# Kernel tuning notes

Measured on AMD Instinct MI355X. Metric: run time of the kernel, lower is better.

Reference implementation:

```python
import jax, jax.numpy as jnp
import numpy as np

B, S, D, M = 8, 32, 256, 2048
TOPK = 8

def setup_inputs() -> dict:
    key = jax.random.key(0)
    ks = jax.random.split(key, 10)
    def lin(kw, fan_in, fan_out):
        # kaiming normal (linear): std = 1/sqrt(fan_in); stored as [in, out]
        return jax.random.normal(kw, (fan_in, fan_out), jnp.float32) / jnp.sqrt(fan_in)
    return {
        "x": jax.random.normal(ks[0], (B, S, D), jnp.float32),
        "memory": jax.random.normal(ks[1], (M, D), jnp.float32) * 0.02,
        "Wq": lin(ks[2], D, D), "bq": jnp.zeros((D,), jnp.float32),
        "Wk": lin(ks[3], D, D), "bk": jnp.zeros((D,), jnp.float32),
        "Wv": lin(ks[4], D, D), "bv": jnp.zeros((D,), jnp.float32),
        "Wg": lin(ks[5], 2 * D, D), "bg": jnp.zeros((D,), jnp.float32),
    }

def reference(x, memory, Wq, bq, Wk, bk, Wv, bv, Wg, bg):
    batch, seq_len, d = x.shape
    scale = jnp.sqrt(jnp.float32(d))
    mem0 = jnp.broadcast_to(memory[None], (batch,) + memory.shape)  # [B,M,D]
    b_idx = jnp.arange(batch)[:, None]

    def step(mem, xt):  # mem [B,M,D], xt [B,D]
        q = xt @ Wq + bq                      # [B,D]
        k = mem @ Wk + bk                     # [B,M,D]
        v = mem @ Wv + bv                     # [B,M,D]
        logits = jnp.einsum('bd,bmd->bm', q, k) / scale
        attn = jax.nn.softmax(logits, axis=-1)            # [B,M]
        out = jnp.einsum('bm,bmd->bd', attn, v)           # [B,D]
        g = jax.nn.sigmoid(jnp.concatenate([xt, out], axis=-1) @ Wg + bg)  # [B,D]
        _, top_idx = jax.lax.top_k(attn, TOPK)            # [B,TOPK]
        old = jnp.take_along_axis(mem, top_idx[:, :, None], axis=1)        # [B,TOPK,D]
        new = (1.0 - g)[:, None, :] * old + g[:, None, :] * xt[:, None, :]
        mem = mem.at[b_idx, top_idx].set(new)
        return mem, out

    _, outs = jax.lax.scan(step, mem0, jnp.swapaxes(x, 0, 1))  # outs [S,B,D]
    return jnp.swapaxes(outs, 0, 1)  # [B,S,D]
```

## Files before the change

### kernel.cpp

```cpp
#include <hip/hip_runtime.h>
#include <math.h>

constexpr int B_ = 8, S_ = 32, D_ = 256, M_ = 2048;
constexpr int N_ = S_ * B_;
constexpr int TK = 8;
constexpr int NSLOT = 256;
constexpr int TOPC = 256;
constexpr int NCAND = NSLOT + TOPC;
constexpr int KSPLIT = 4;
constexpr int CACHE0 = 192;

__global__ __launch_bounds__(256) void k_wvwgT(const float* __restrict__ Wv,
                                               const float* __restrict__ Wg,
                                               const float* __restrict__ bv,
                                               const float* __restrict__ bg,
                                               const float* __restrict__ Wk,
                                               float* __restrict__ WvWgB,
                                               float* __restrict__ bvg,
                                               float* __restrict__ WkT) {
  int blk = blockIdx.x;
  int tid = threadIdx.x;
  if (blk >= 17) {
    __shared__ float tile[32][33];
    int bb = blk - 17;
    int bx = bb & 7, by = bb >> 3;
    int x0 = bx * 32, y0 = by * 32;
    int tx = tid & 31, ty = tid >> 5;
    for (int j = ty; j < 32; j += 8) tile[j][tx] = Wk[(y0 + j) * D_ + x0 + tx];
    __syncthreads();
    for (int j = ty; j < 32; j += 8) WkT[(x0 + j) * D_ + y0 + tx] = tile[tx][j];
    return;
  }
  if (blk == 16) {
    float a = bg[tid];
#pragma unroll 8
    for (int j = 0; j < D_; ++j) a = fmaf(bv[j], Wg[(size_t)(D_ + j) * D_ + tid], a);
    bvg[tid] = a;
    return;
  }
  int i0 = (blk & 3) * 64, d0 = (blk >> 2) * 64;
  __shared__ float At[64 * 64];
  __shared__ float Bt[64 * 64];
  const int r = tid & 63, c = tid >> 6;
  const int lane = tid & 63, wvv = tid >> 6;
  const int tx = lane & 15, ty = lane >> 4;
  const int dg = tx * 4, ig = (wvv * 4 + ty) * 4;
  float acc[4][4];
#pragma unroll
  for (int i = 0; i < 4; ++i)
#pragma unroll
    for (int j = 0; j < 4; ++j) acc[i][j] = 0.f;
  for (int kc = 0; kc < 4; ++kc) {
    __syncthreads();
#pragma unroll
    for (int it = 0; it < 4; ++it) {
      int jq = (c * 4 + it) * 4;
      float4 a = *(const float4*)&Wv[(i0 + r) * D_ + kc * 64 + jq];
      At[(jq + 0) * 64 + r] = a.x; At[(jq + 1) * 64 + r] = a.y;
      At[(jq + 2) * 64 + r] = a.z; At[(jq + 3) * 64 + r] = a.w;
      *(float4*)&Bt[r * 64 + jq] =
          *(const float4*)&Wg[(size_t)(D_ + kc * 64 + r) * D_ + d0 + jq];
    }
    __syncthreads();
#pragma unroll 4
    for (int j = 0; j < 64; ++j) {
      float4 av = *(const float4*)&At[j * 64 + ig];
      float4 bv4 = *(const float4*)&Bt[j * 64 + dg];
      acc[0][0] = fmaf(av.x, bv4.x, acc[0][0]); acc[0][1] = fmaf(av.x, bv4.y, acc[0][1]);
      acc[0][2] = fmaf(av.x, bv4.z, acc[0][2]); acc[0][3] = fmaf(av.x, bv4.w, acc[0][3]);
      acc[1][0] = fmaf(av.y, bv4.x, acc[1][0]); acc[1][1] = fmaf(av.y, bv4.y, acc[1][1]);
      acc[1][2] = fmaf(av.y, bv4.z, acc[1][2]); acc[1][3] = fmaf(av.y, bv4.w, acc[1][3]);
      acc[2][0] = fmaf(av.z, bv4.x, acc[2][0]); acc[2][1] = fmaf(av.z, bv4.y, acc[2][1]);
      acc[2][2] = fmaf(av.z, bv4.z, acc[2][2]); acc[2][3] = fmaf(av.z, bv4.w, acc[2][3]);
      acc[3][0] = fmaf(av.w, bv4.x, acc[3][0]); acc[3][1] = fmaf(av.w, bv4.y, acc[3][1]);
      acc[3][2] = fmaf(av.w, bv4.z, acc[3][2]); acc[3][3] = fmaf(av.w, bv4.w, acc[3][3]);
    }
  }
#pragma unroll
  for (int i = 0; i < 4; ++i)
    *(float4*)&WvWgB[(size_t)(i0 + ig + i) * D_ + d0 + dg] =
        make_float4(acc[i][0], acc[i][1], acc[i][2], acc[i][3]);
}

__global__ __launch_bounds__(256) void k_qproj(
    const float* __restrict__ x, const float* __restrict__ Wq,
    const float* __restrict__ bq, const float* __restrict__ bk,
    const float* __restrict__ WkT, const float* __restrict__ Wg,
    float* __restrict__ qt, float* __restrict__ qbk, float* __restrict__ xgp) {
  int n = blockIdx.x, tid = threadIdx.x;
  int t = n / B_, b = n % B_;
  __shared__ float xr[D_], qsh[D_];
  __shared__ float red[4];
  xr[tid] = x[(b * S_ + t) * D_ + tid];
  __syncthreads();
  float accq = bq[tid], accg = 0.f;
#pragma unroll 8
  for (int i = 0; i < D_; ++i) {
    float xv = xr[i];
    accq = fmaf(xv, Wq[i * D_ + tid], accq);
    accg = fmaf(xv, Wg[i * D_ + tid], accg);
  }
  qsh[tid] = accq;
  xgp[n * D_ + tid] = accg;
  float p = accq * bk[tid];
  for (int off = 32; off > 0; off >>= 1) p += __shfl_down(p, off, 64);
  if ((tid & 63) == 0) red[tid >> 6] = p;
  __syncthreads();
  float acct = 0.f;
#pragma unroll 8
  for (int i = 0; i < D_; ++i) acct = fmaf(qsh[i], WkT[i * D_ + tid], acct);
  qt[n * D_ + tid] = acct;
  if (tid == 0) qbk[n] = red[0] + red[1] + red[2] + red[3];
}

__global__ __launch_bounds__(256) void k_L0(
    const float* __restrict__ qt, const float* __restrict__ mem,
    const float* __restrict__ qbk, float* __restrict__ L0) {
  __shared__ float qtT[64 * 64];
  __shared__ float mT[64 * 64];
  const int tid = threadIdx.x;
  const int m0 = blockIdx.x * 64, n0 = blockIdx.y * 64;
  const int r = tid & 63, c = tid >> 6;
  const int lane = tid & 63, wv = tid >> 6;
  const int tx = lane & 15, ty = lane >> 4;
  const int mg = tx * 4, ng = (wv * 4 + ty) * 4;
  float acc[4][4];
#pragma unroll
  for (int i = 0; i < 4; ++i)
#pragma unroll
    for (int j = 0; j < 4; ++j) acc[i][j] = 0.f;
  for (int kc = 0; kc < 4; ++kc) {
    __syncthreads();
#pragma unroll
    for (int it = 0; it < 4; ++it) {
      int kq = (c * 4 + it) * 4;
      float4 a = *(const float4*)&qt[(n0 + r) * D_ + kc * 64 + kq];
      qtT[(kq + 0) * 64 + r] = a.x; qtT[(kq + 1) * 64 + r] = a.y;
      qtT[(kq + 2) * 64 + r] = a.z; qtT[(kq + 3) * 64 + r] = a.w;
      float4 bm = *(const float4*)&mem[(m0 + r) * D_ + kc * 64 + kq];
      mT[(kq + 0) * 64 + r] = bm.x; mT[(kq + 1) * 64 + r] = bm.y;
      mT[(kq + 2) * 64 + r] = bm.z; mT[(kq + 3) * 64 + r] = bm.w;
    }
    __syncthreads();
#pragma unroll 4
    for (int k = 0; k < 64; ++k) {
      float4 av = *(const float4*)&qtT[k * 64 + ng];
      float4 bv4 = *(const float4*)&mT[k * 64 + mg];
      acc[0][0] = fmaf(av.x, bv4.x, acc[0][0]); acc[0][1] = fmaf(av.x, bv4.y, acc[0][1]);
      acc[0][2] = fmaf(av.x, bv4.z, acc[0][2]); acc[0][3] = fmaf(av.x, bv4.w, acc[0][3]);
      acc[1][0] = fmaf(av.y, bv4.x, acc[1][0]); acc[1][1] = fmaf(av.y, bv4.y, acc[1][1]);
      acc[1][2] = fmaf(av.y, bv4.z, acc[1][2]); acc[1][3] = fmaf(av.y, bv4.w, acc[1][3]);
      acc[2][0] = fmaf(av.z, bv4.x, acc[2][0]); acc[2][1] = fmaf(av.z, bv4.y, acc[2][1]);
      acc[2][2] = fmaf(av.z, bv4.z, acc[2][2]); acc[2][3] = fmaf(av.z, bv4.w, acc[2][3]);
      acc[3][0] = fmaf(av.w, bv4.x, acc[3][0]); acc[3][1] = fmaf(av.w, bv4.y, acc[3][1]);
      acc[3][2] = fmaf(av.w, bv4.z, acc[3][2]); acc[3][3] = fmaf(av.w, bv4.w, acc[3][3]);
    }
  }
#pragma unroll
  for (int i = 0; i < 4; ++i) {
    int n = n0 + ng + i;
    float qbv = qbk[n];
    float4 o;
    o.x = (acc[i][0] + qbv) * 0.0625f; o.y = (acc[i][1] + qbv) * 0.0625f;
    o.z = (acc[i][2] + qbv) * 0.0625f; o.w = (acc[i][3] + qbv) * 0.0625f;
    *(float4*)&L0[n * M_ + m0 + mg] = o;
  }
}

__global__ __launch_bounds__(1024) void k_sortstats(const float* __restrict__ L0,
                                                    float* __restrict__ topv,
                                                    int* __restrict__ topi,
                                                    float* __restrict__ M0,
                                                    double* __restrict__ SumE0) {
  int n = blockIdx.x, tid = threadIdx.x;
  __shared__ float v[M_];
  __shared__ short ix[M_];
  __shared__ double redd[16];
  for (int m = tid; m < M_; m += 1024) {
    v[m] = L0[(size_t)n * M_ + m];
    ix[m] = (short)m;
  }
  __syncthreads();
  for (int size = 2; size <= M_; size <<= 1) {
    for (int stride = size >> 1; stride > 0; stride >>= 1) {
      const int i = tid;
      const int pos = 2 * i - (i & (stride - 1));
      const int j = pos + stride;
      const bool desc = ((pos & size) == 0);
      const float va = v[pos], vb2 = v[j];
      const short ia = ix[pos], ib = ix[j];
      const bool aG = (va > vb2) || (va == vb2 && ia < ib);
      if (desc ? !aG : aG) { v[pos] = vb2; v[j] = va; ix[pos] = ib; ix[j] = ia; }
      __syncthreads();
    }
  }
  if (tid < TOPC) {
    topv[n * TOPC + tid] = v[tid];
    topi[n * TOPC + tid] = (int)ix[tid];
  }
  float mx = v[0];
  if (tid == 0) M0[n] = mx;
  double s = 0.0;
  for (int m = tid; m < M_; m += 1024) s += (double)expf(v[m] - mx);
  for (int off = 32; off > 0; off >>= 1) s += __shfl_down(s, off, 64);
  if ((tid & 63) == 0) redd[tid >> 6] = s;
  __syncthreads();
  if (tid == 0) {
    double t = 0.0;
#pragma unroll
    for (int w = 0; w < 16; ++w) t += redd[w];
    SumE0[n] = t;
  }
}

__global__ __launch_bounds__(256) void k_ctxpart(
    const float* __restrict__ L0, const float* __restrict__ M0,
    const float* __restrict__ mem, float* __restrict__ ctxp) {
  int ks = blockIdx.x;
  int n0 = blockIdx.y * 32;
  int d0 = blockIdx.z * 64;
  int tid = threadIdx.x;
  __shared__ float Et[64 * 32];
  __shared__ float mTl[64 * 64];
  __shared__ float Msh[32];
  if (tid < 32) Msh[tid] = M0[n0 + tid];
  const int lane = tid & 63, wv = tid >> 6;
  const int tx = lane & 15, ty = lane >> 4;
  const int ng = (wv * 4 + ty) * 2;
  const int dg = tx * 4;
  float acc[2][4] = {{0, 0, 0, 0}, {0, 0, 0, 0}};
  for (int kc = 0; kc < 8; ++kc) {
    int kb = ks * 512 + kc * 64;
    __syncthreads();
#pragma unroll
    for (int j = 0; j < 8; ++j) {
      int ii = tid + 256 * j;
      int nr = ii & 31, kk = ii >> 5;
      Et[kk * 32 + nr] = expf(L0[(n0 + nr) * M_ + kb + kk] - Msh[nr]);
    }
    {
      int r = tid & 63, c = tid >> 6;
#pragma unroll
      for (int j = 0; j < 4; ++j) {
        int c4 = (c * 4 + j) * 4;
        *(float4*)&mTl[r * 64 + c4] = *(const float4*)&mem[(kb + r) * D_ + d0 + c4];
      }
    }
    __syncthreads();
#pragma unroll 4
    for (int kk = 0; kk < 64; ++kk) {
      float4 mv = *(const float4*)&mTl[kk * 64 + dg];
      float e0v = Et[kk * 32 + ng], e1v = Et[kk * 32 + ng + 1];
      acc[0][0] = fmaf(e0v, mv.x, acc[0][0]); acc[0][1] = fmaf(e0v, mv.y, acc[0][1]);
      acc[0][2] = fmaf(e0v, mv.z, acc[0][2]); acc[0][3] = fmaf(e0v, mv.w, acc[0][3]);
      acc[1][0] = fmaf(e1v, mv.x, acc[1][0]); acc[1][1] = fmaf(e1v, mv.y, acc[1][1]);
      acc[1][2] = fmaf(e1v, mv.z, acc[1][2]); acc[1][3] = fmaf(e1v, mv.w, acc[1][3]);
    }
  }
#pragma unroll
  for (int i = 0; i < 2; ++i) {
    int n = n0 + ng + i;
    *(float4*)&ctxp[((size_t)ks * N_ + n) * D_ + d0 + dg] =
        make_float4(acc[i][0], acc[i][1], acc[i][2], acc[i][3]);
  }
}

__device__ __forceinline__ unsigned long long shfl_xor_u64(unsigned long long v,
                                                           int off) {
  const int lo = __shfl_xor((int)(unsigned)(v & 0xFFFFFFFFull), off, 64);
  const int hi = __shfl_xor((int)(unsigned)(v >> 32), off, 64);
  return ((unsigned long long)(unsigned)hi << 32) | (unsigned)lo;
}

#define CE8(i, jj)                                                  \
  {                                                                 \
    const unsigned long long ka_ = key[i], kb_ = key[jj];           \
    const bool sw_ = kb_ > ka_;                                     \
    key[i] = sw_ ? kb_ : ka_;                                       \
    key[jj] = sw_ ? ka_ : kb_;                                      \
  }

__global__ __launch_bounds__(1024, 4) void k_scan(
    const float* __restrict__ x, const float* __restrict__ mem0,
    const float* __restrict__ Wv, const float* __restrict__ bv,
    const float* __restrict__ WvWgB, const float* __restrict__ bvg,
    const float* __restrict__ qt, const float* __restrict__ qbk,
    const float* __restrict__ xgp, const float* __restrict__ L0,
    const float* __restrict__ M0, const double* __restrict__ SumE0,
    const float* __restrict__ ctxp, const float* __restrict__ topv,
    const int* __restrict__ topi, float* __restrict__ memcur,
    float* __restrict__ out) {
  const int b = blockIdx.x;
  const int tid = threadIdx.x;
  const int lane = tid & 63;
  const int wvid = tid >> 6;

  __shared__ short tpos[M_];
  __shared__ unsigned int descL[NSLOT];
  __shared__ __align__(16) float candV[NCAND];
  __shared__ __align__(16) int candI[NCAND];
  __shared__ float diffA[NSLOT];
  __shared__ float dpart[15][D_];
  __shared__ float fpart[15][D_];
  __shared__ float fpart2[15][D_];
  __shared__ float qt_s[2][D_], xt_s[2][D_];
  __shared__ float CTX0_s[D_], xgp_s[D_], g_s[D_], bv_s[D_], bvg_s[D_];
  __shared__ float wvlds[(256 - CACHE0) * D_];
  __shared__ float Msc[S_], qbks[S_];
  __shared__ double sum0s[S_];
  __shared__ float inv_esum;
  __shared__ int Tcount;

  const float4* mem04 = (const float4*)mem0;
  const float4* mcur4c = (const float4*)memcur;
  float4* mcur4 = (float4*)memcur;
  const float4* Wv4 = (const float4*)Wv;
  const float4* Wg4 = (const float4*)WvWgB;
  const float4* qt4 = (const float4*)qt;
  const float4* x4 = (const float4*)x;
  const float4* ctxp4 = (const float4*)ctxp;
  const float4* xgp4 = (const float4*)xgp;
  const float4* wvlds4 = (const float4*)wvlds;

  float4 wreg[18];
  {
    const int kbase = 17 * wvid;
    if (wvid < 15) {
#pragma unroll
      for (int j = 0; j < 17; ++j) wreg[j] = Wv4[(size_t)(kbase + j) * 64 + lane];
      wreg[17] = (wvid == 14) ? Wv4[(size_t)255 * 64 + lane] : wreg[16];
    }
  }

  for (int m = tid; m < M_; m += 1024) tpos[m] = -1;
  for (int s = tid; s < NSLOT; s += 1024) descL[s] = 0;
  for (int i = tid; i < (256 - CACHE0) * 64; i += 1024)
    ((float4*)wvlds)[i] = Wg4[(size_t)CACHE0 * 64 + i];
  if (tid < NCAND) {
    candV[tid] = -INFINITY;
    candI[tid] = 0x7FFFFFFF;
  }
  if (tid < S_) {
    Msc[tid] = M0[tid * B_ + b];
    qbks[tid] = qbk[tid * B_ + b];
    sum0s[tid] = SumE0[tid * B_ + b];
  } else if (tid >= 64 && tid < 64 + D_) {
    int d = tid - 64;
    bv_s[d] = bv[d];
    bvg_s[d] = bvg[d];
  } else if (tid >= 512 && tid < 576) {
    int j = tid - 512;
    ((float4*)qt_s[0])[j] = qt4[(size_t)b * 64 + j];
  } else if (tid >= 576 && tid < 640) {
    int j = tid - 576;
    ((float4*)xt_s[0])[j] = x4[(size_t)(b * S_) * 64 + j];
  }
  if (tid == 0) Tcount = 0;
  __syncthreads();

  for (int t = 0; t < S_; ++t) {
    const int n = t * B_ + b;
    const int par = t & 1;
    const int Tc = Tcount;
    const float c0 = Msc[t];
    const float qb = qbks[t];

    if (wvid < 15) {
      const float4 qv = ((const float4*)qt_s[par])[lane];
      const float4 g4 = ((const float4*)g_s)[lane];
      const float4 xpv = ((const float4*)xt_s[par ^ 1])[lane];
      float4 acc = make_float4(0.f, 0.f, 0.f, 0.f);
      int s = wvid;
      unsigned int dsc_c = 0;
      float4 mc_c = make_float4(0.f, 0.f, 0.f, 0.f), mo_c = mc_c;
      float l0_c = 0.f;
      if (s < Tc) {
        dsc_c = descL[s];
        const int m = dsc_c & 2047;
        mo_c = mem04[(size_t)m * 64 + lane];
        const bool fromM0 = (dsc_c & (1u << 12)) && (dsc_c & (1u << 11));
        mc_c = fromM0 ? mo_c : mcur4c[(size_t)(b * NSLOT + s) * 64 + lane];
        l0_c = L0[(size_t)n * M_ + m];
      }
      while (s < Tc) {
        const int s2 = s + 15;
        unsigned int dsc_n = 0;
        float4 mc_n = make_float4(0.f, 0.f, 0.f, 0.f), mo_n = mc_n;
        float l0_n = 0.f;
        if (s2 < Tc) {
          dsc_n = descL[s2];
          const int mn = dsc_n & 2047;
          mo_n = mem04[(size_t)mn * 64 + lane];
          const bool fromM0n = (dsc_n & (1u << 12)) && (dsc_n & (1u << 11));
          mc_n = fromM0n ? mo_n : mcur4c[(size_t)(b * NSLOT + s2) * 64 + lane];
          l0_n = L0[(size_t)n * M_ + mn];
        }
        const int m = dsc_c & 2047;
        if (dsc_c & (1u << 12)) {
          mc_c.x = fmaf(g4.x, xpv.x - mc_c.x, mc_c.x);
          mc_c.y = fmaf(g4.y, xpv.y - mc_c.y, mc_c.y);
          mc_c.z = fmaf(g4.z, xpv.z - mc_c.z, mc_c.z);
          mc_c.w = fmaf(g4.w, xpv.w - mc_c.w, mc_c.w);
          mcur4[(size_t)(b * NSLOT + s) * 64 + lane] = mc_c;
          if (lane == 0) descL[s] = (unsigned int)m;
        }
        float p = mc_c.x * qv.x;
        p = fmaf(mc_c.y, qv.y, p);
        p = fmaf(mc_c.z, qv.z, p);
        p = fmaf(mc_c.w, qv.w, p);
#pragma unroll
        for (int off = 1; off < 64; off <<= 1) p += __shfl_xor(p, off, 64);
        const float cur = (p + qb) * 0.0625f;
        const float ce = expf(cur - c0);
        const float e0 = expf(l0_c - c0);
        acc.x = fmaf(ce, mc_c.x, fmaf(-e0, mo_c.x, acc.x));
        acc.y = fmaf(ce, mc_c.y, fmaf(-e0, mo_c.y, acc.y));
        acc.z = fmaf(ce, mc_c.z, fmaf(-e0, mo_c.z, acc.z));
        acc.w = fmaf(ce, mc_c.w, fmaf(-e0, mo_c.w, acc.w));
        if (lane == 0) {
          diffA[s] = ce - e0;
          candV[s] = cur;
          candI[s] = m;
        }
        dsc_c = dsc_n;
        mc_c = mc_n;
        mo_c = mo_n;
        l0_c = l0_n;
        s = s2;
      }
      ((float4*)dpart[wvid])[lane] = acc;
    } else {
#pragma unroll
      for (int jj = 0; jj < 4; ++jj) {
        const int j = lane + jj * 64;
        const int ii = topi[n * TOPC + j];
        const bool fresh = (tpos[ii] < 0);
        candV[NSLOT + j] = fresh ? topv[n * TOPC + j] : -INFINITY;
        candI[NSLOT + j] = fresh ? ii : 0x7FFFFFFF;
      }
      const float4 c0v = ctxp4[(size_t)(0 * N_ + n) * 64 + lane];
      const float4 c1v = ctxp4[(size_t)(1 * N_ + n) * 64 + lane];
      const float4 c2v = ctxp4[(size_t)(2 * N_ + n) * 64 + lane];
      const float4 c3v = ctxp4[(size_t)(3 * N_ + n) * 64 + lane];
      ((float4*)CTX0_s)[lane] = make_float4(c0v.x + c1v.x + c2v.x + c3v.x,
                                            c0v.y + c1v.y + c2v.y + c3v.y,
                                            c0v.z + c1v.z + c2v.z + c3v.z,
                                            c0v.w + c1v.w + c2v.w + c3v.w);
      ((float4*)xgp_s)[lane] = xgp4[(size_t)n * 64 + lane];
      if (t + 1 < S_) {
        ((float4*)qt_s[par ^ 1])[lane] = qt4[(size_t)(n + B_) * 64 + lane];
        ((float4*)xt_s[par ^ 1])[lane] = x4[(size_t)(b * S_ + t + 1) * 64 + lane];
      }
    }
    __syncthreads();

    if (wvid < 15) {
      const int kbase = 17 * wvid;
      const int nr = (wvid == 14) ? 18 : 17;
      float mynum = 0.f;
      if (lane < nr) {
        const int k = (lane == 17) ? 255 : (kbase + lane);
        float nv = CTX0_s[k];
#pragma unroll
        for (int p = 0; p < 15; ++p) nv += dpart[p][k];
        mynum = nv;
      }
      float4 a1 = make_float4(0.f, 0.f, 0.f, 0.f);
      float4 a2 = make_float4(0.f, 0.f, 0.f, 0.f);
#pragma unroll
      for (int j = 0; j < 17; ++j) {
        const float nv = __int_as_float(__builtin_amdgcn_readlane(__float_as_int(mynum), j));
        a1.x = fmaf(nv, wreg[j].x, a1.x); a1.y = fmaf(nv, wreg[j].y, a1.y);
        a1.z = fmaf(nv, wreg[j].z, a1.z); a1.w = fmaf(nv, wreg[j].w, a1.w);
        const int r = kbase + j;
        const float4 w4 = (r >= CACHE0) ? wvlds4[(size_t)(r - CACHE0) * 64 + lane]
                                        : Wg4[(size_t)r * 64 + lane];
        a2.x = fmaf(nv, w4.x, a2.x); a2.y = fmaf(nv, w4.y, a2.y);
        a2.z = fmaf(nv, w4.z, a2.z); a2.w = fmaf(nv, w4.w, a2.w);
      }
      if (wvid == 14) {
        const float nv = __int_as_float(__builtin_amdgcn_readlane(__float_as_int(mynum), 17));
        a1.x = fmaf(nv, wreg[17].x, a1.x); a1.y = fmaf(nv, wreg[17].y, a1.y);
        a1.z = fmaf(nv, wreg[17].z, a1.z); a1.w = fmaf(nv, wreg[17].w, a1.w);
        const float4 w4 = wvlds4[(size_t)(255 - CACHE0) * 64 + lane];
        a2.x = fmaf(nv, w4.x, a2.x); a2.y = fmaf(nv, w4.y, a2.y);
        a2.z = fmaf(nv, w4.z, a2.z); a2.w = fmaf(nv, w4.w, a2.w);
      }
      ((float4*)fpart[wvid])[lane] = a1;
      ((float4*)fpart2[wvid])[lane] = a2;
      if (wvid == 0) {
        double dsum = 0.0;
        for (int s2 = lane; s2 < Tc; s2 += 64) dsum += (double)diffA[s2];
#pragma unroll
        for (int off = 32; off > 0; off >>= 1) dsum += __shfl_down(dsum, off, 64);
        if (lane == 0) inv_esum = (float)(1.0 / (sum0s[t] + dsum));
      }
    } else if (t + 1 < S_) {
      const float4 cv0 = ((const float4*)candV)[lane * 2];
      const float4 cv1 = ((const float4*)candV)[lane * 2 + 1];
      const int4 ci0 = ((const int4*)candI)[lane * 2];
      const int4 ci1 = ((const int4*)candI)[lane * 2 + 1];
      unsigned long long key[8];
      {
        const float vs[8] = {cv0.x, cv0.y, cv0.z, cv0.w, cv1.x, cv1.y, cv1.z, cv1.w};
        const int is[8] = {ci0.x, ci0.y, ci0.z, ci0.w, ci1.x, ci1.y, ci1.z, ci1.w};
#pragma unroll
        for (int j = 0; j < 8; ++j) {
          unsigned int bits = __float_as_uint(vs[j]);
          bits = (bits & 0x80000000u) ? ~bits : (bits | 0x80000000u);
          key[j] = ((unsigned long long)bits << 11) |
                   (unsigned long long)(2047 - (is[j] & 2047));
        }
      }
      CE8(0, 1) CE8(2, 3) CE8(4, 5) CE8(6, 7)
      CE8(0, 2) CE8(1, 3) CE8(4, 6) CE8(5, 7)
      CE8(1, 2) CE8(5, 6)
      CE8(0, 4) CE8(1, 5) CE8(2, 6) CE8(3, 7)
      CE8(2, 4) CE8(3, 5)
      CE8(1, 2) CE8(3, 4) CE8(5, 6)
#pragma unroll
      for (int off = 1; off < 64; off <<= 1) {
        unsigned long long pk[8];
#pragma unroll
        for (int j = 0; j < 8; ++j) pk[j] = shfl_xor_u64(key[7 - j], off);
#pragma unroll
        for (int j = 0; j < 8; ++j) key[j] = (pk[j] > key[j]) ? pk[j] : key[j];
        CE8(0, 4) CE8(1, 5) CE8(2, 6) CE8(3, 7)
        CE8(0, 2) CE8(1, 3) CE8(4, 6) CE8(5, 7)
        CE8(0, 1) CE8(2, 3) CE8(4, 5) CE8(6, 7)
      }
      int myM = 2047 - (int)(key[0] & 2047);
#pragma unroll
      for (int r = 1; r < TK; ++r) {
        const int mr = 2047 - (int)(key[r] & 2047);
        if (lane == r) myM = mr;
      }
      int sOld = 0;
      bool fresh = false;
      if (lane < TK) {
        sOld = (int)tpos[myM];
        fresh = sOld < 0;
      }
      const unsigned long long fm = __ballot(fresh);
      if (lane < TK) {
        const int before = (int)__popcll(fm & ((1ull << lane) - 1ull));
        const int snew = fresh ? (Tc + before) : sOld;
        if (fresh) {
          tpos[myM] = (short)snew;
          candI[snew] = myM;
        }
        descL[snew] = (unsigned int)myM | ((fresh ? 1u : 0u) << 11) | (1u << 12);
      }
      if (lane == 0) Tcount = Tc + (int)__popcll(fm);
    }
    __syncthreads();

    if (tid < D_) {
      float o = 0.f;
#pragma unroll
      for (int p = 0; p < 15; ++p) o += fpart[p][tid];
      o = o * inv_esum + bv_s[tid];
      out[((size_t)b * S_ + t) * D_ + tid] = o;
    } else if (tid < 2 * D_) {
      const int d = tid - D_;
      float gg = 0.f;
#pragma unroll
      for (int p = 0; p < 15; ++p) gg += fpart2[p][d];
      const float gin = xgp_s[d] + gg * inv_esum + bvg_s[d];
      g_s[d] = 1.0f / (1.0f + expf(-gin));
    }
    __syncthreads();
  }
}

extern "C" void kernel_launch(void* const* d_in, const int* in_sizes, int n_in,
                              void* d_out, int out_size, void* d_ws, size_t ws_size,
                              hipStream_t stream) {
  const float* x = (const float*)d_in[0];
  const float* mem0 = (const float*)d_in[1];
  const float* Wq = (const float*)d_in[2];
  const float* bq = (const float*)d_in[3];
  const float* Wk = (const float*)d_in[4];
  const float* bk = (const float*)d_in[5];
  const float* Wv = (const float*)d_in[6];
  const float* bv = (const float*)d_in[7];
  const float* Wg = (const float*)d_in[8];
  const float* bg = (const float*)d_in[9];
  float* out = (float*)d_out;
  float* ws = (float*)d_ws;

  size_t o = 0;
  float* WkT = ws + o;    o += (size_t)D_ * D_;
  float* qt = ws + o;     o += (size_t)N_ * D_;
  float* qbk = ws + o;    o += N_;
  float* xgp = ws + o;    o += (size_t)N_ * D_;
  float* L0 = ws + o;     o += (size_t)N_ * M_;
  float* M0 = ws + o;     o += N_;
  double* SumE0 = (double*)(ws + o); o += 2 * N_;
  float* ctxp = ws + o;   o += (size_t)KSPLIT * N_ * D_;
  float* topv = ws + o;   o += (size_t)N_ * TOPC;
  int* topi = (int*)(ws + o); o += (size_t)N_ * TOPC;
  float* WvWgB = ws + o;  o += (size_t)D_ * D_;
  float* bvg = ws + o;    o += D_;
  float* memcur = ws + o; o += (size_t)B_ * NSLOT * D_;

  k_wvwgT<<<dim3(81), dim3(256), 0, stream>>>(Wv, Wg, bv, bg, Wk, WvWgB, bvg, WkT);
  k_qproj<<<dim3(N_), dim3(256), 0, stream>>>(x, Wq, bq, bk, WkT, Wg, qt, qbk, xgp);
  k_L0<<<dim3(M_ / 64, N_ / 64), dim3(256), 0, stream>>>(qt, mem0, qbk, L0);
  k_sortstats<<<dim3(N_), dim3(1024), 0, stream>>>(L0, topv, topi, M0, SumE0);
  k_ctxpart<<<dim3(KSPLIT, N_ / 32, D_ / 64), dim3(256), 0, stream>>>(L0, M0, mem0, ctxp);
  k_scan<<<dim3(B_), dim3(1024), 0, stream>>>(x, mem0, Wv, bv, WvWgB, bvg, qt, qbk, xgp,
                                              L0, M0, SumE0, ctxp, topv, topi, memcur, out);
}
```

Measured before the change: 606.0 us.

## Defer output and gate reductions into next step to drop a barrier

Removes the trailing per-step reduction phase and its __syncthreads. Each of the 15 compute waves now recomputes the sigmoid gate redundantly from fpart2 at the start of the next step. The 16th wave writes the previous step's output while it loads the next inputs, and a final epilogue writes the last timestep. xgp_s is double-buffered so the gate can use the previous step's values. This saves one block-wide barrier per timestep in exchange for redundant gate work in every wave and possible hazards on shared buffers reused across steps.

Measured after the change: 615.8 us. Within noise of the previous version (+1.6%).

```diff
diff --git a/kernel.cpp b/kernel.cpp
--- a/kernel.cpp
+++ b/kernel.cpp
@@ -304,7 +304,8 @@
   __shared__ float fpart[15][D_];
   __shared__ float fpart2[15][D_];
   __shared__ float qt_s[2][D_], xt_s[2][D_];
-  __shared__ float CTX0_s[D_], xgp_s[D_], g_s[D_], bv_s[D_], bvg_s[D_];
+  __shared__ float xgp_s[2][D_];
+  __shared__ float CTX0_s[D_], bv_s[D_], bvg_s[D_];
   __shared__ float wvlds[(256 - CACHE0) * D_];
   __shared__ float Msc[S_], qbks[S_];
   __shared__ double sum0s[S_];
@@ -366,8 +367,27 @@
     const float qb = qbks[t];
 
     if (wvid < 15) {
+      float4 g4 = make_float4(0.f, 0.f, 0.f, 0.f);
+      if (t > 0) {
+        float4 gg = make_float4(0.f, 0.f, 0.f, 0.f);
+#pragma unroll
+        for (int p = 0; p < 15; ++p) {
+          const float4 f2 = ((const float4*)fpart2[p])[lane];
+          gg.x += f2.x; gg.y += f2.y; gg.z += f2.z; gg.w += f2.w;
+        }
+        const float ie = inv_esum;
+        const float4 xg = ((const float4*)xgp_s[par ^ 1])[lane];
+        const float4 bg4 = ((const float4*)bvg_s)[lane];
+        const float4 gin = make_float4(xg.x + gg.x * ie + bg4.x,
+                                       xg.y + gg.y * ie + bg4.y,
+                                       xg.z + gg.z * ie + bg4.z,
+                                       xg.w + gg.w * ie + bg4.w);
+        g4.x = 1.0f / (1.0f + expf(-gin.x));
+        g4.y = 1.0f / (1.0f + expf(-gin.y));
+        g4.z = 1.0f / (1.0f + expf(-gin.z));
+        g4.w = 1.0f / (1.0f + expf(-gin.w));
+      }
       const float4 qv = ((const float4*)qt_s[par])[lane];
-      const float4 g4 = ((const float4*)g_s)[lane];
       const float4 xpv = ((const float4*)xt_s[par ^ 1])[lane];
       float4 acc = make_float4(0.f, 0.f, 0.f, 0.f);
       int s = wvid;
@@ -430,6 +450,20 @@
       }
       ((float4*)dpart[wvid])[lane] = acc;
     } else {
+      if (t > 0) {
+        float4 oa = make_float4(0.f, 0.f, 0.f, 0.f);
+#pragma unroll
+        for (int p = 0; p < 15; ++p) {
+          const float4 f1 = ((const float4*)fpart[p])[lane];
+          oa.x += f1.x; oa.y += f1.y; oa.z += f1.z; oa.w += f1.w;
+        }
+        const float ie = inv_esum;
+        const float4 bv4 = ((const float4*)bv_s)[lane];
+        float4 o;
+        o.x = oa.x * ie + bv4.x; o.y = oa.y * ie + bv4.y;
+        o.z = oa.z * ie + bv4.z; o.w = oa.w * ie + bv4.w;
+        *(float4*)&out[((size_t)b * S_ + (t - 1)) * D_ + lane * 4] = o;
+      }
 #pragma unroll
       for (int jj = 0; jj < 4; ++jj) {
         const int j = lane + jj * 64;
@@ -446,7 +480,7 @@
                                             c0v.y + c1v.y + c2v.y + c3v.y,
                                             c0v.z + c1v.z + c2v.z + c3v.z,
                                             c0v.w + c1v.w + c2v.w + c3v.w);
-      ((float4*)xgp_s)[lane] = xgp4[(size_t)n * 64 + lane];
+      ((float4*)xgp_s[par])[lane] = xgp4[(size_t)n * 64 + lane];
       if (t + 1 < S_) {
         ((float4*)qt_s[par ^ 1])[lane] = qt4[(size_t)(n + B_) * 64 + lane];
         ((float4*)xt_s[par ^ 1])[lane] = x4[(size_t)(b * S_ + t + 1) * 64 + lane];
@@ -554,22 +588,21 @@
       if (lane == 0) Tcount = Tc + (int)__popcll(fm);
     }
     __syncthreads();
-
-    if (tid < D_) {
-      float o = 0.f;
-#pragma unroll
-      for (int p = 0; p < 15; ++p) o += fpart[p][tid];
-      o = o * inv_esum + bv_s[tid];
-      out[((size_t)b * S_ + t) * D_ + tid] = o;
-    } else if (tid < 2 * D_) {
-      const int d = tid - D_;
-      float gg = 0.f;
-#pragma unroll
-      for (int p = 0; p < 15; ++p) gg += fpart2[p][d];
-      const float gin = xgp_s[d] + gg * inv_esum + bvg_s[d];
-      g_s[d] = 1.0f / (1.0f + expf(-gin));
-    }
-    __syncthreads();
+  }
+
+  if (wvid == 15) {
+    float4 oa = make_float4(0.f, 0.f, 0.f, 0.f);
+#pragma unroll
+    for (int p = 0; p < 15; ++p) {
+      const float4 f1 = ((const float4*)fpart[p])[lane];
+      oa.x += f1.x; oa.y += f1.y; oa.z += f1.z; oa.w += f1.w;
+    }
+    const float ie = inv_esum;
+    const float4 bv4 = ((const float4*)bv_s)[lane];
+    float4 o;
+    o.x = oa.x * ie + bv4.x; o.y = oa.y * ie + bv4.y;
+    o.z = oa.z * ie + bv4.z; o.w = oa.w * ie + bv4.w;
+    *(float4*)&out[((size_t)b * S_ + (S_ - 1)) * D_ + lane * 4] = o;
   }
 }
 
```

## Process four slots per wave in touched-slot loop, drop Wv register cache, use fast exp

Applied to the files above, without the earlier changes.

The per-step loop over touched memory slots changes shape. Each wave now splits into four 16-lane groups, and each group handles one slot with 16 floats per lane. The dot-product reduction shrinks to 16 lanes, with one cross-group reduction of the accumulators at the end. This replaces the one-slot-per-iteration loop that used a full 64-lane shuffle reduction and a software prefetch. The 18 float4 Wv registers are no longer preloaded and are re-read from global memory each step, which frees registers but adds global traffic. expf is swapped for __expf throughout, trading a little accuracy for cheaper exponentials.

After: 688.3 us. 13.6% more time.

```diff
diff --git a/kernel.cpp b/kernel.cpp
--- a/kernel.cpp
+++ b/kernel.cpp
@@ -201,7 +201,7 @@
   float mx = v[0];
   if (tid == 0) M0[n] = mx;
   double s = 0.0;
-  for (int m = tid; m < M_; m += 1024) s += (double)expf(v[m] - mx);
+  for (int m = tid; m < M_; m += 1024) s += (double)__expf(v[m] - mx);
   for (int off = 32; off > 0; off >>= 1) s += __shfl_down(s, off, 64);
   if ((tid & 63) == 0) redd[tid >> 6] = s;
   __syncthreads();
@@ -236,7 +236,7 @@
     for (int j = 0; j < 8; ++j) {
       int ii = tid + 256 * j;
       int nr = ii & 31, kk = ii >> 5;
-      Et[kk * 32 + nr] = expf(L0[(n0 + nr) * M_ + kb + kk] - Msh[nr]);
+      Et[kk * 32 + nr] = __expf(L0[(n0 + nr) * M_ + kb + kk] - Msh[nr]);
     }
     {
       int r = tid & 63, c = tid >> 6;
@@ -322,16 +322,6 @@
   const float4* xgp4 = (const float4*)xgp;
   const float4* wvlds4 = (const float4*)wvlds;
 
-  float4 wreg[18];
-  {
-    const int kbase = 17 * wvid;
-    if (wvid < 15) {
-#pragma unroll
-      for (int j = 0; j < 17; ++j) wreg[j] = Wv4[(size_t)(kbase + j) * 64 + lane];
-      wreg[17] = (wvid == 14) ? Wv4[(size_t)255 * 64 + lane] : wreg[16];
-    }
-  }
-
   for (int m = tid; m < M_; m += 1024) tpos[m] = -1;
   for (int s = tid; s < NSLOT; s += 1024) descL[s] = 0;
   for (int i = tid; i < (256 - CACHE0) * 64; i += 1024)
@@ -366,69 +356,119 @@
     const float qb = qbks[t];
 
     if (wvid < 15) {
-      const float4 qv = ((const float4*)qt_s[par])[lane];
-      const float4 g4 = ((const float4*)g_s)[lane];
-      const float4 xpv = ((const float4*)xt_s[par ^ 1])[lane];
-      float4 acc = make_float4(0.f, 0.f, 0.f, 0.f);
-      int s = wvid;
-      unsigned int dsc_c = 0;
-      float4 mc_c = make_float4(0.f, 0.f, 0.f, 0.f), mo_c = mc_c;
-      float l0_c = 0.f;
-      if (s < Tc) {
-        dsc_c = descL[s];
-        const int m = dsc_c & 2047;
-        mo_c = mem04[(size_t)m * 64 + lane];
-        const bool fromM0 = (dsc_c & (1u << 12)) && (dsc_c & (1u << 11));
-        mc_c = fromM0 ? mo_c : mcur4c[(size_t)(b * NSLOT + s) * 64 + lane];
-        l0_c = L0[(size_t)n * M_ + m];
-      }
-      while (s < Tc) {
-        const int s2 = s + 15;
-        unsigned int dsc_n = 0;
-        float4 mc_n = make_float4(0.f, 0.f, 0.f, 0.f), mo_n = mc_n;
-        float l0_n = 0.f;
-        if (s2 < Tc) {
-          dsc_n = descL[s2];
-          const int mn = dsc_n & 2047;
-          mo_n = mem04[(size_t)mn * 64 + lane];
-          const bool fromM0n = (dsc_n & (1u << 12)) && (dsc_n & (1u << 11));
-          mc_n = fromM0n ? mo_n : mcur4c[(size_t)(b * NSLOT + s2) * 64 + lane];
-          l0_n = L0[(size_t)n * M_ + mn];
+      const int grp = lane >> 4;
+      const int u = lane & 15;
+      float4 qr0 = ((const float4*)qt_s[par])[u * 4 + 0];
+      float4 qr1 = ((const float4*)qt_s[par])[u * 4 + 1];
+      float4 qr2 = ((const float4*)qt_s[par])[u * 4 + 2];
+      float4 qr3 = ((const float4*)qt_s[par])[u * 4 + 3];
+      float4 acc0 = make_float4(0.f, 0.f, 0.f, 0.f);
+      float4 acc1 = acc0, acc2 = acc0, acc3 = acc0;
+      const int nown = (Tc > wvid) ? ((Tc - wvid + 14) / 15) : 0;
+      for (int j0 = 0; j0 < 17; j0 += 4) {
+        if (j0 >= nown) break;
+        const int j = j0 + grp;
+        const bool act = (j < nown);
+        const int s = act ? (wvid + 15 * j) : 0;
+        const unsigned int dsc = act ? descL[s] : 0u;
+        const int m = dsc & 2047;
+        const size_t mobase = (size_t)m * 64 + u * 4;
+        const size_t mcbase = (size_t)(b * NSLOT + s) * 64 + u * 4;
+        float l0v = 0.f;
+        float4 mc0, mc1, mc2, mc3;
+        float e0 = 0.f;
+        if (act) {
+          l0v = L0[(size_t)n * M_ + m];
+          const bool fromM0 = (dsc & (1u << 12)) && (dsc & (1u << 11));
+          const float4 mo0 = mem04[mobase + 0];
+          const float4 mo1 = mem04[mobase + 1];
+          const float4 mo2 = mem04[mobase + 2];
+          const float4 mo3 = mem04[mobase + 3];
+          if (fromM0) {
+            mc0 = mo0; mc1 = mo1; mc2 = mo2; mc3 = mo3;
+          } else {
+            mc0 = mcur4c[mcbase + 0];
+            mc1 = mcur4c[mcbase + 1];
+            mc2 = mcur4c[mcbase + 2];
+            mc3 = mcur4c[mcbase + 3];
+          }
+          if (dsc & (1u << 12)) {
+            const float4 g0 = ((const float4*)g_s)[u * 4 + 0];
+            const float4 g1 = ((const float4*)g_s)[u * 4 + 1];
+            const float4 g2 = ((const float4*)g_s)[u * 4 + 2];
+            const float4 g3 = ((const float4*)g_s)[u * 4 + 3];
+            const float4 xp0 = ((const float4*)xt_s[par ^ 1])[u * 4 + 0];
+            const float4 xp1 = ((const float4*)xt_s[par ^ 1])[u * 4 + 1];
+            const float4 xp2 = ((const float4*)xt_s[par ^ 1])[u * 4 + 2];
+            const float4 xp3 = ((const float4*)xt_s[par ^ 1])[u * 4 + 3];
+            mc0.x = fmaf(g0.x, xp0.x - mc0.x, mc0.x); mc0.y = fmaf(g0.y, xp0.y - mc0.y, mc0.y);
+            mc0.z = fmaf(g0.z, xp0.z - mc0.z, mc0.z); mc0.w = fmaf(g0.w, xp0.w - mc0.w, mc0.w);
+            mc1.x = fmaf(g1.x, xp1.x - mc1.x, mc1.x); mc1.y = fmaf(g1.y, xp1.y - mc1.y, mc1.y);
+            mc1.z = fmaf(g1.z, xp1.z - mc1.z, mc1.z); mc1.w = fmaf(g1.w, xp1.w - mc1.w, mc1.w);
+            mc2.x = fmaf(g2.x, xp2.x - mc2.x, mc2.x); mc2.y = fmaf(g2.y, xp2.y - mc2.y, mc2.y);
+            mc2.z = fmaf(g2.z, xp2.z - mc2.z, mc2.z); mc2.w = fmaf(g2.w, xp2.w - mc2.w, mc2.w);
+            mc3.x = fmaf(g3.x, xp3.x - mc3.x, mc3.x); mc3.y = fmaf(g3.y, xp3.y - mc3.y, mc3.y);
+            mc3.z = fmaf(g3.z, xp3.z - mc3.z, mc3.z); mc3.w = fmaf(g3.w, xp3.w - mc3.w, mc3.w);
+            mcur4[mcbase + 0] = mc0; mcur4[mcbase + 1] = mc1;
+            mcur4[mcbase + 2] = mc2; mcur4[mcbase + 3] = mc3;
+            if (u == 0) descL[s] = (unsigned int)m;
+          }
+          e0 = __expf(l0v - c0);
+          acc0.x = fmaf(-e0, mo0.x, acc0.x); acc0.y = fmaf(-e0, mo0.y, acc0.y);
+          acc0.z = fmaf(-e0, mo0.z, acc0.z); acc0.w = fmaf(-e0, mo0.w, acc0.w);
+          acc1.x = fmaf(-e0, mo1.x, acc1.x); acc1.y = fmaf(-e0, mo1.y, acc1.y);
+          acc1.z = fmaf(-e0, mo1.z, acc1.z); acc1.w = fmaf(-e0, mo1.w, acc1.w);
+          acc2.x = fmaf(-e0, mo2.x, acc2.x); acc2.y = fmaf(-e0, mo2.y, acc2.y);
+          acc2.z = fmaf(-e0, mo2.z, acc2.z); acc2.w = fmaf(-e0, mo2.w, acc2.w);
+          acc3.x = fmaf(-e0, mo3.x, acc3.x); acc3.y = fmaf(-e0, mo3.y, acc3.y);
+          acc3.z = fmaf(-e0, mo3.z, acc3.z); acc3.w = fmaf(-e0, mo3.w, acc3.w);
+        } else {
+          mc0 = make_float4(0.f, 0.f, 0.f, 0.f);
+          mc1 = mc0; mc2 = mc0; mc3 = mc0;
         }
-        const int m = dsc_c & 2047;
-        if (dsc_c & (1u << 12)) {
-          mc_c.x = fmaf(g4.x, xpv.x - mc_c.x, mc_c.x);
-          mc_c.y = fmaf(g4.y, xpv.y - mc_c.y, mc_c.y);
-          mc_c.z = fmaf(g4.z, xpv.z - mc_c.z, mc_c.z);
-          mc_c.w = fmaf(g4.w, xpv.w - mc_c.w, mc_c.w);
-          mcur4[(size_t)(b * NSLOT + s) * 64 + lane] = mc_c;
-          if (lane == 0) descL[s] = (unsigned int)m;
-        }
-        float p = mc_c.x * qv.x;
-        p = fmaf(mc_c.y, qv.y, p);
-        p = fmaf(mc_c.z, qv.z, p);
-        p = fmaf(mc_c.w, qv.w, p);
-#pragma unroll
-        for (int off = 1; off < 64; off <<= 1) p += __shfl_xor(p, off, 64);
+        float p = mc0.x * qr0.x;
+        p = fmaf(mc0.y, qr0.y, p); p = fmaf(mc0.z, qr0.z, p); p = fmaf(mc0.w, qr0.w, p);
+        p = fmaf(mc1.x, qr1.x, p); p = fmaf(mc1.y, qr1.y, p);
+        p = fmaf(mc1.z, qr1.z, p); p = fmaf(mc1.w, qr1.w, p);
+        p = fmaf(mc2.x, qr2.x, p); p = fmaf(mc2.y, qr2.y, p);
+        p = fmaf(mc2.z, qr2.z, p); p = fmaf(mc2.w, qr2.w, p);
+        p = fmaf(mc3.x, qr3.x, p); p = fmaf(mc3.y, qr3.y, p);
+        p = fmaf(mc3.z, qr3.z, p); p = fmaf(mc3.w, qr3.w, p);
+#pragma unroll
+        for (int off = 1; off < 16; off <<= 1) p += __shfl_xor(p, off, 64);
         const float cur = (p + qb) * 0.0625f;
-        const float ce = expf(cur - c0);
-        const float e0 = expf(l0_c - c0);
-        acc.x = fmaf(ce, mc_c.x, fmaf(-e0, mo_c.x, acc.x));
-        acc.y = fmaf(ce, mc_c.y, fmaf(-e0, mo_c.y, acc.y));
-        acc.z = fmaf(ce, mc_c.z, fmaf(-e0, mo_c.z, acc.z));
-        acc.w = fmaf(ce, mc_c.w, fmaf(-e0, mo_c.w, acc.w));
-        if (lane == 0) {
+        const float ce = act ? __expf(cur - c0) : 0.f;
+        acc0.x = fmaf(ce, mc0.x, acc0.x); acc0.y = fmaf(ce, mc0.y, acc0.y);
+        acc0.z = fmaf(ce, mc0.z, acc0.z); acc0.w = fmaf(ce, mc0.w, acc0.w);
+        acc1.x = fmaf(ce, mc1.x, acc1.x); acc1.y = fmaf(ce, mc1.y, acc1.y);
+        acc1.z = fmaf(ce, mc1.z, acc1.z); acc1.w = fmaf(ce, mc1.w, acc1.w);
+        acc2.x = fmaf(ce, mc2.x, acc2.x); acc2.y = fmaf(ce, mc2.y, acc2.y);
+        acc2.z = fmaf(ce, mc2.z, acc2.z); acc2.w = fmaf(ce, mc2.w, acc2.w);
+        acc3.x = fmaf(ce, mc3.x, acc3.x); acc3.y = fmaf(ce, mc3.y, acc3.y);
+        acc3.z = fmaf(ce, mc3.z, acc3.z); acc3.w = fmaf(ce, mc3.w, acc3.w);
+        if (act && u == 0) {
           diffA[s] = ce - e0;
           candV[s] = cur;
           candI[s] = m;
         }
-        dsc_c = dsc_n;
-        mc_c = mc_n;
-        mo_c = mo_n;
-        l0_c = l0_n;
-        s = s2;
-      }
-      ((float4*)dpart[wvid])[lane] = acc;
+      }
+#pragma unroll
+      for (int off = 16; off < 64; off <<= 1) {
+        acc0.x += __shfl_xor(acc0.x, off, 64); acc0.y += __shfl_xor(acc0.y, off, 64);
+        acc0.z += __shfl_xor(acc0.z, off, 64); acc0.w += __shfl_xor(acc0.w, off, 64);
+        acc1.x += __shfl_xor(acc1.x, off, 64); acc1.y += __shfl_xor(acc1.y, off, 64);
+        acc1.z += __shfl_xor(acc1.z, off, 64); acc1.w += __shfl_xor(acc1.w, off, 64);
+        acc2.x += __shfl_xor(acc2.x, off, 64); acc2.y += __shfl_xor(acc2.y, off, 64);
+        acc2.z += __shfl_xor(acc2.z, off, 64); acc2.w += __shfl_xor(acc2.w, off, 64);
+        acc3.x += __shfl_xor(acc3.x, off, 64); acc3.y += __shfl_xor(acc3.y, off, 64);
+        acc3.z += __shfl_xor(acc3.z, off, 64); acc3.w += __shfl_xor(acc3.w, off, 64);
+      }
+      if (grp == 0) {
+        ((float4*)dpart[wvid])[u * 4 + 0] = acc0;
+        ((float4*)dpart[wvid])[u * 4 + 1] = acc1;
+        ((float4*)dpart[wvid])[u * 4 + 2] = acc2;
+        ((float4*)dpart[wvid])[u * 4 + 3] = acc3;
+      }
     } else {
 #pragma unroll
       for (int jj = 0; jj < 4; ++jj) {
@@ -470,9 +510,10 @@
 #pragma unroll
       for (int j = 0; j < 17; ++j) {
         const float nv = __int_as_float(__builtin_amdgcn_readlane(__float_as_int(mynum), j));
-        a1.x = fmaf(nv, wreg[j].x, a1.x); a1.y = fmaf(nv, wreg[j].y, a1.y);
-        a1.z = fmaf(nv, wreg[j].z, a1.z); a1.w = fmaf(nv, wreg[j].w, a1.w);
         const int r = kbase + j;
+        const float4 wv4 = Wv4[(size_t)r * 64 + lane];
+        a1.x = fmaf(nv, wv4.x, a1.x); a1.y = fmaf(nv, wv4.y, a1.y);
+        a1.z = fmaf(nv, wv4.z, a1.z); a1.w = fmaf(nv, wv4.w, a1.w);
         const float4 w4 = (r >= CACHE0) ? wvlds4[(size_t)(r - CACHE0) * 64 + lane]
                                         : Wg4[(size_t)r * 64 + lane];
         a2.x = fmaf(nv, w4.x, a2.x); a2.y = fmaf(nv, w4.y, a2.y);
@@ -480,8 +521,9 @@
       }
       if (wvid == 14) {
         const float nv = __int_as_float(__builtin_amdgcn_readlane(__float_as_int(mynum), 17));
-        a1.x = fmaf(nv, wreg[17].x, a1.x); a1.y = fmaf(nv, wreg[17].y, a1.y);
-        a1.z = fmaf(nv, wreg[17].z, a1.z); a1.w = fmaf(nv, wreg[17].w, a1.w);
+        const float4 wv4 = Wv4[(size_t)255 * 64 + lane];
+        a1.x = fmaf(nv, wv4.x, a1.x); a1.y = fmaf(nv, wv4.y, a1.y);
+        a1.z = fmaf(nv, wv4.z, a1.z); a1.w = fmaf(nv, wv4.w, a1.w);
         const float4 w4 = wvlds4[(size_t)(255 - CACHE0) * 64 + lane];
         a2.x = fmaf(nv, w4.x, a2.x); a2.y = fmaf(nv, w4.y, a2.y);
         a2.z = fmaf(nv, w4.z, a2.z); a2.w = fmaf(nv, w4.w, a2.w);
@@ -567,7 +609,7 @@
 #pragma unroll
       for (int p = 0; p < 15; ++p) gg += fpart2[p][d];
       const float gin = xgp_s[d] + gg * inv_esum + bvg_s[d];
-      g_s[d] = 1.0f / (1.0f + expf(-gin));
+      g_s[d] = 1.0f / (1.0f + __expf(-gin));
     }
     __syncthreads();
   }
```
